# Kernel optimization log

Hardware: AMD Instinct MI355X
Metric: run time of the kernel (lower is better)

## Reference

```python
import jax, jax.numpy as jnp
import numpy as np

B, N, C, DK, TOPK = 4, 4096, 256, 64, 8


def setup_inputs() -> dict:
    key = jax.random.key(0)
    k1, k2, k3 = jax.random.split(key, 3)
    x = jax.random.normal(k1, (B, N, C), dtype=jnp.float32)
    # nn.Linear(channels, d_k, bias=False) weights, stored as [C, DK] for x @ W
    W_q = jax.random.normal(k2, (C, DK), dtype=jnp.float32) * (C ** -0.5)
    W_k = jax.random.normal(k3, (C, DK), dtype=jnp.float32) * (C ** -0.5)
    return {"x": x, "W_q": W_q, "W_k": W_k, "top_k": TOPK}


def reference(x, W_q, W_k, top_k):
    d_k = W_q.shape[-1]
    scale = d_k ** -0.5
    Q = x @ W_q                                   # [B, N, DK]
    K = x @ W_k                                   # [B, N, DK]
    S = jnp.einsum('bnd,bmd->bnm', Q, K) * scale  # [B, N, N]
    _, topk_idx = jax.lax.top_k(S, top_k)         # [B, N, top_k]
    n = S.shape[-1]
    # scatter True at top-k column indices per row (mirrors torch scatter_)
    row_mask = lambda idx: jnp.zeros((n,), dtype=bool).at[idx].set(True)
    mask = jax.vmap(jax.vmap(row_mask))(topk_idx)  # [B, N, N] bool
    S_masked = jnp.where(mask, S, -jnp.inf)
    A = jax.nn.softmax(S_masked, axis=-1)
    return A
```

## Files before the change

### kernel.cpp

```cpp
#include <hip/hip_runtime.h>
#include <math.h>

#define NROW 16384
#define NCOL 4096
#define CDIM 256
#define DKDIM 64
#define SCALE 0.125f

typedef float v4f __attribute__((ext_vector_type(4)));
typedef __attribute__((ext_vector_type(8))) short short8v;
typedef __attribute__((ext_vector_type(4))) float f32x4;

__device__ __forceinline__ unsigned mono(float v) {
  unsigned u = __float_as_uint(v);
  unsigned s = (unsigned)(((int)u) >> 31);
  return u ^ (s | 0x80000000u);
}
__device__ __forceinline__ float unmono(unsigned k) {
  unsigned u = (k & 0x80000000u) ? (k ^ 0x80000000u) : ~k;
  return __uint_as_float(u);
}
__device__ __forceinline__ unsigned short f2bf(float f) {
  unsigned u = __float_as_uint(f);
  u += 0x7FFFu + ((u >> 16) & 1u);
  return (unsigned short)(u >> 16);
}
__device__ __forceinline__ unsigned umaxu(unsigned a, unsigned b) { return a > b ? a : b; }

__device__ __forceinline__ void ins8(unsigned tk[8], unsigned& tmin, int& tmpos, unsigned v) {
  #pragma unroll
  for (int j = 0; j < 8; ++j) if (j == tmpos) tk[j] = v;
  tmin = tk[0]; tmpos = 0;
  #pragma unroll
  for (int j = 1; j < 8; ++j) if (tk[j] < tmin) { tmin = tk[j]; tmpos = j; }
}
__device__ __forceinline__ unsigned umax8(const unsigned kv[8]) {
  unsigned a = umaxu(umaxu(kv[0], kv[1]), umaxu(kv[2], kv[3]));
  unsigned b = umaxu(umaxu(kv[4], kv[5]), umaxu(kv[6], kv[7]));
  return umaxu(a, b);
}
__device__ __forceinline__ void seed8(const unsigned* __restrict__ sp,
                                      unsigned tk[8], unsigned& tmin, int& tmpos) {
  uint4 ka = *(const uint4*)(sp);
  uint4 kb = *(const uint4*)(sp + 4);
  tk[0] = ka.x; tk[1] = ka.y; tk[2] = ka.z; tk[3] = ka.w;
  tk[4] = kb.x; tk[5] = kb.y; tk[6] = kb.z; tk[7] = kb.w;
  tmin = tk[0]; tmpos = 0;
  #pragma unroll
  for (int j = 1; j < 8; ++j) if (tk[j] < tmin) { tmin = tk[j]; tmpos = j; }
}
__device__ __forceinline__ void scan8(const unsigned* __restrict__ sp,
                                      unsigned tk[8], unsigned& tmin, int& tmpos) {
  uint4 ka = *(const uint4*)(sp);
  uint4 kb = *(const uint4*)(sp + 4);
  unsigned kv[8] = {ka.x, ka.y, ka.z, ka.w, kb.x, kb.y, kb.z, kb.w};
  unsigned gm = umax8(kv);
  #pragma unroll
  for (int pass = 0; pass < 2; ++pass) {
    if (__any(gm > tmin)) {
      if (gm > tmin) {
        ins8(tk, tmin, tmpos, gm);
        #pragma unroll
        for (int j = 0; j < 8; ++j) if (kv[j] == gm) kv[j] = 0u;
      }
      gm = umax8(kv);
    }
  }
  if (__any(gm > tmin)) {
    #pragma unroll
    for (int j = 0; j < 8; ++j) if (kv[j] > tmin) ins8(tk, tmin, tmpos, kv[j]);
  }
}

__global__ __launch_bounds__(512, 2) void qk_proj(
    const float* __restrict__ x, const float* __restrict__ Wq,
    const float* __restrict__ Wk, float* __restrict__ Qt,
    float* __restrict__ Kt, unsigned short* __restrict__ Qh,
    unsigned short* __restrict__ Kh) {
  __shared__ float4 xs4[64][65];
  const int t = threadIdx.x;
  const int rb = blockIdx.x;
  {
    const float4* xg = (const float4*)(x + (size_t)rb * 64 * CDIM);
    #pragma unroll
    for (int i = 0; i < 8; ++i) {
      int idx = i * 512 + t;
      xs4[idx >> 6][idx & 63] = xg[idx];
    }
  }
  __syncthreads();

  const int lane = t & 63;
  const int wu = __builtin_amdgcn_readfirstlane(t >> 6);
  const int proj = wu >> 2;
  const int chunk = wu & 3;
  const float* __restrict__ Wp = proj ? Wk : Wq;

  float acc[16];
  #pragma unroll
  for (int j = 0; j < 16; ++j) acc[j] = 0.f;

  #pragma unroll 4
  for (int cs = 0; cs < 64; ++cs) {
    float4 xv = xs4[lane][cs];
    const float xc[4] = {xv.x, xv.y, xv.z, xv.w};
    #pragma unroll
    for (int i = 0; i < 4; ++i) {
      const float4* __restrict__ w4 =
          (const float4*)(Wp + (size_t)(cs * 4 + i) * DKDIM + chunk * 16);
      float4 wa = w4[0], wb = w4[1], wc = w4[2], wd = w4[3];
      float xi = xc[i];
      acc[0]  = fmaf(xi, wa.x, acc[0]);  acc[1]  = fmaf(xi, wa.y, acc[1]);
      acc[2]  = fmaf(xi, wa.z, acc[2]);  acc[3]  = fmaf(xi, wa.w, acc[3]);
      acc[4]  = fmaf(xi, wb.x, acc[4]);  acc[5]  = fmaf(xi, wb.y, acc[5]);
      acc[6]  = fmaf(xi, wb.z, acc[6]);  acc[7]  = fmaf(xi, wb.w, acc[7]);
      acc[8]  = fmaf(xi, wc.x, acc[8]);  acc[9]  = fmaf(xi, wc.y, acc[9]);
      acc[10] = fmaf(xi, wc.z, acc[10]); acc[11] = fmaf(xi, wc.w, acc[11]);
      acc[12] = fmaf(xi, wd.x, acc[12]); acc[13] = fmaf(xi, wd.y, acc[13]);
      acc[14] = fmaf(xi, wd.z, acc[14]); acc[15] = fmaf(xi, wd.w, acc[15]);
    }
  }

  const int gr = rb * 64 + lane;
  float* Of = (proj ? Kt : Qt) + (size_t)gr * 64 + chunk * 16;
  #pragma unroll
  for (int i = 0; i < 4; ++i) {
    float4 o = {acc[4 * i], acc[4 * i + 1], acc[4 * i + 2], acc[4 * i + 3]};
    ((float4*)Of)[i] = o;
  }
  unsigned short* Oh = (proj ? Kh : Qh) + (size_t)gr * 64 + chunk * 16;
  unsigned hp[8];
  #pragma unroll
  for (int i = 0; i < 8; ++i)
    hp[i] = (unsigned)f2bf(acc[2 * i]) | ((unsigned)f2bf(acc[2 * i + 1]) << 16);
  uint4 h0 = {hp[0], hp[1], hp[2], hp[3]};
  uint4 h1 = {hp[4], hp[5], hp[6], hp[7]};
  ((uint4*)Oh)[0] = h0;
  ((uint4*)Oh)[1] = h1;
}

__global__ __launch_bounds__(256, 4) void s_cand(
    const unsigned short* __restrict__ Qh, const unsigned short* __restrict__ Kh,
    float* __restrict__ out, unsigned* __restrict__ wsk) {
  __shared__ unsigned keys[4][16 * 132];
  const int t = threadIdx.x;
  const int lane = t & 63;
  const int w = __builtin_amdgcn_readfirstlane(t >> 6);
  const int f = blockIdx.x;
  const int xs = f & 7;
  const int i5 = f >> 3;
  const int combo = xs * 4 + (i5 >> 6);
  const int rbL = i5 & 63;
  const int b = combo >> 3;
  const int chunk = combo & 7;
  const int rb = b * 64 + rbL;

  const int l15 = lane & 15, lk = lane >> 4;
  const int rowg = (b << 12) + rbL * 64 + w * 16 + l15;
  const short8v a0 = *(const short8v*)(Qh + (size_t)rowg * 64 + lk * 8);
  const short8v a1 = *(const short8v*)(Qh + (size_t)rowg * 64 + lk * 8 + 32);

  {
    v4f z = {0.f, 0.f, 0.f, 0.f};
    v4f* o4 = (v4f*)out + (size_t)rb * 64 * 1024 + chunk * 128;
    #pragma unroll 8
    for (int i = 0; i < 32; ++i) {
      int g = i * 256 + t;
      __builtin_nontemporal_store(z, &o4[(size_t)(g >> 7) * 1024 + (g & 127)]);
    }
  }

  unsigned* krow = keys[w];
  const int myrow = lane >> 2, q = lane & 3;
  const unsigned short* Kb = Kh + ((size_t)(b << 12)) * 64;

  unsigned tk[8]; unsigned tmin; int tmpos;

  #pragma unroll 1
  for (int qt = 0; qt < 4; ++qt) {
    const int colbase = chunk * 512 + qt * 128;
    #pragma unroll
    for (int ct = 0; ct < 8; ++ct) {
      const int col = colbase + ct * 16 + l15;
      const unsigned short* kp = Kb + (size_t)col * 64 + lk * 8;
      const short8v b0 = *(const short8v*)(kp);
      const short8v b1 = *(const short8v*)(kp + 32);
      f32x4 acc = {0.f, 0.f, 0.f, 0.f};
      acc = __builtin_amdgcn_mfma_f32_16x16x32_bf16(a0, b0, acc, 0, 0, 0);
      acc = __builtin_amdgcn_mfma_f32_16x16x32_bf16(a1, b1, acc, 0, 0, 0);
      #pragma unroll
      for (int i = 0; i < 4; ++i) {
        unsigned kk = (mono(acc[i]) & 0xFFFFF000u) | (unsigned)col;
        krow[(lk * 4 + i) * 132 + ct * 16 + l15] = kk;
      }
    }
    const unsigned* sp = krow + myrow * 132 + q * 32;
    if (qt == 0) {
      seed8(sp, tk, tmin, tmpos);
      scan8(sp + 8, tk, tmin, tmpos);
      scan8(sp + 16, tk, tmin, tmpos);
      scan8(sp + 24, tk, tmin, tmpos);
    } else {
      #pragma unroll
      for (int g = 0; g < 4; ++g) scan8(sp + 8 * g, tk, tmin, tmpos);
    }
  }

  {
    uint4 s0 = {tk[0], tk[1], tk[2], tk[3]};
    uint4 s1 = {tk[4], tk[5], tk[6], tk[7]};
    uint4* mp4 = (uint4*)(krow + myrow * 36 + q * 8);
    mp4[0] = s0; mp4[1] = s1;
  }
  if (lane < 16) {
    const unsigned* mp = krow + lane * 36;
    unsigned mt[8]; unsigned mmin; int mmpos;
    seed8(mp, mt, mmin, mmpos);
    scan8(mp + 8, mt, mmin, mmpos);
    scan8(mp + 16, mt, mmin, mmpos);
    scan8(mp + 24, mt, mmin, mmpos);
    const int grow = (b << 12) + rbL * 64 + w * 16 + lane;
    uint4 o0 = {mt[0], mt[1], mt[2], mt[3]};
    uint4 o1 = {mt[4], mt[5], mt[6], mt[7]};
    uint4* wp = (uint4*)(wsk + (size_t)grow * 64 + chunk * 8);
    wp[0] = o0; wp[1] = o1;
  }
}

__global__ __launch_bounds__(256) void finalize(
    const float* __restrict__ Qt, const float* __restrict__ Kt,
    const unsigned* __restrict__ wsk, float* __restrict__ out) {
  const int t = threadIdx.x;
  const int lane = t & 63;
  const int w = t >> 6;
  const int row = blockIdx.x * 4 + w;
  const int b = row >> 12;
  const unsigned key = wsk[(size_t)row * 64 + lane];
  const int col = (int)(key & 0xFFFu);
  const float4* Kp = (const float4*)(Kt + ((size_t)((b << 12) + col)) * 64);
  const float4* Qp = (const float4*)(Qt + (size_t)row * 64);
  float s = 0.f;
  #pragma unroll
  for (int g = 0; g < 16; ++g) {
    float4 qf = Qp[g];
    float4 kf = Kp[g];
    s = fmaf(qf.x, kf.x, s);
    s = fmaf(qf.y, kf.y, s);
    s = fmaf(qf.z, kf.z, s);
    s = fmaf(qf.w, kf.w, s);
  }
  unsigned kx = mono(s);
  float vals[8]; int cols[8];
  #pragma unroll
  for (int it = 0; it < 8; ++it) {
    unsigned m = kx;
    #pragma unroll
    for (int d = 1; d < 64; d <<= 1) m = umaxu(m, (unsigned)__shfl_xor((int)m, d, 64));
    unsigned long long win = __ballot(kx == m);
    int wl = (int)__ffsll(win) - 1;
    cols[it] = __shfl(col, wl, 64);
    vals[it] = unmono(m);
    if (lane == wl) kx = 0u;
  }
  float e[8], sum = 0.f;
  #pragma unroll
  for (int it = 0; it < 8; ++it) { e[it] = __expf((vals[it] - vals[0]) * SCALE); sum += e[it]; }
  float inv = 1.f / sum;
  if (lane == 0) {
    float* orow = out + ((size_t)row << 12);
    #pragma unroll
    for (int it = 0; it < 8; ++it) orow[cols[it]] = e[it] * inv;
  }
}

extern "C" void kernel_launch(void* const* d_in, const int* in_sizes, int n_in,
                              void* d_out, int out_size, void* d_ws, size_t ws_size,
                              hipStream_t stream) {
  const float* x  = (const float*)d_in[0];
  const float* Wq = (const float*)d_in[1];
  const float* Wk = (const float*)d_in[2];
  float* out = (float*)d_out;

  char* ws = (char*)d_ws;
  float* Qt = (float*)ws;
  float* Kt = (float*)(ws + ((size_t)4 << 20));
  unsigned short* Qh = (unsigned short*)(ws + ((size_t)8 << 20));
  unsigned short* Kh = (unsigned short*)(ws + ((size_t)10 << 20));
  unsigned* wsk = (unsigned*)(ws + ((size_t)12 << 20));

  qk_proj<<<dim3(NROW / 64), 512, 0, stream>>>(x, Wq, Wk, Qt, Kt, Qh, Kh);
  s_cand<<<2048, 256, 0, stream>>>(Qh, Kh, out, wsk);
  finalize<<<NROW / 4, 256, 0, stream>>>(Qt, Kt, wsk, out);
}
```

Measured before the change: 467.9 us.

## Move output zero-fill into projection kernel and keep top-k candidates in registers

The zero-fill of the 256MB output moves from the candidate kernel into the projection kernel, where it is interleaved with the FMA loop. The idea is that the write traffic overlaps compute in a kernel that is not bandwidth-bound. The candidate kernel now keeps per-row top-8 state in registers for each of the 4 MFMA output rows, instead of staging every score key through LDS and scanning. A two-level LDS merge follows at the end. The cost is higher register pressure in s_cand, and qk_proj becomes dominated by the fill.

```diff
diff --git a/kernel.cpp b/kernel.cpp
--- a/kernel.cpp
+++ b/kernel.cpp
@@ -39,21 +39,19 @@
   unsigned b = umaxu(umaxu(kv[4], kv[5]), umaxu(kv[6], kv[7]));
   return umaxu(a, b);
 }
-__device__ __forceinline__ void seed8(const unsigned* __restrict__ sp,
-                                      unsigned tk[8], unsigned& tmin, int& tmpos) {
-  uint4 ka = *(const uint4*)(sp);
-  uint4 kb = *(const uint4*)(sp + 4);
-  tk[0] = ka.x; tk[1] = ka.y; tk[2] = ka.z; tk[3] = ka.w;
-  tk[4] = kb.x; tk[5] = kb.y; tk[6] = kb.z; tk[7] = kb.w;
+__device__ __forceinline__ void seed8r(const unsigned kv[8],
+                                       unsigned tk[8], unsigned& tmin, int& tmpos) {
+  #pragma unroll
+  for (int j = 0; j < 8; ++j) tk[j] = kv[j];
   tmin = tk[0]; tmpos = 0;
   #pragma unroll
   for (int j = 1; j < 8; ++j) if (tk[j] < tmin) { tmin = tk[j]; tmpos = j; }
 }
-__device__ __forceinline__ void scan8(const unsigned* __restrict__ sp,
-                                      unsigned tk[8], unsigned& tmin, int& tmpos) {
-  uint4 ka = *(const uint4*)(sp);
-  uint4 kb = *(const uint4*)(sp + 4);
-  unsigned kv[8] = {ka.x, ka.y, ka.z, ka.w, kb.x, kb.y, kb.z, kb.w};
+__device__ __forceinline__ void scan8r(const unsigned kvin[8],
+                                       unsigned tk[8], unsigned& tmin, int& tmpos) {
+  unsigned kv[8];
+  #pragma unroll
+  for (int j = 0; j < 8; ++j) kv[j] = kvin[j];
   unsigned gm = umax8(kv);
   #pragma unroll
   for (int pass = 0; pass < 2; ++pass) {
@@ -71,12 +69,26 @@
     for (int j = 0; j < 8; ++j) if (kv[j] > tmin) ins8(tk, tmin, tmpos, kv[j]);
   }
 }
+__device__ __forceinline__ void seed8(const unsigned* __restrict__ sp,
+                                      unsigned tk[8], unsigned& tmin, int& tmpos) {
+  uint4 ka = *(const uint4*)(sp);
+  uint4 kb = *(const uint4*)(sp + 4);
+  unsigned kv[8] = {ka.x, ka.y, ka.z, ka.w, kb.x, kb.y, kb.z, kb.w};
+  seed8r(kv, tk, tmin, tmpos);
+}
+__device__ __forceinline__ void scan8(const unsigned* __restrict__ sp,
+                                      unsigned tk[8], unsigned& tmin, int& tmpos) {
+  uint4 ka = *(const uint4*)(sp);
+  uint4 kb = *(const uint4*)(sp + 4);
+  unsigned kv[8] = {ka.x, ka.y, ka.z, ka.w, kb.x, kb.y, kb.z, kb.w};
+  scan8r(kv, tk, tmin, tmpos);
+}
 
 __global__ __launch_bounds__(512, 2) void qk_proj(
     const float* __restrict__ x, const float* __restrict__ Wq,
     const float* __restrict__ Wk, float* __restrict__ Qt,
     float* __restrict__ Kt, unsigned short* __restrict__ Qh,
-    unsigned short* __restrict__ Kh) {
+    unsigned short* __restrict__ Kh, float* __restrict__ out) {
   __shared__ float4 xs4[64][65];
   const int t = threadIdx.x;
   const int rb = blockIdx.x;
@@ -96,12 +108,20 @@
   const int chunk = wu & 3;
   const float* __restrict__ Wp = proj ? Wk : Wq;
 
+  v4f* __restrict__ ofill = (v4f*)out + (size_t)rb * 65536;
+  const v4f z = {0.f, 0.f, 0.f, 0.f};
+
   float acc[16];
   #pragma unroll
   for (int j = 0; j < 16; ++j) acc[j] = 0.f;
 
   #pragma unroll 4
   for (int cs = 0; cs < 64; ++cs) {
+    {
+      int g0 = cs * 1024 + t;
+      __builtin_nontemporal_store(z, &ofill[g0]);
+      __builtin_nontemporal_store(z, &ofill[g0 + 512]);
+    }
     float4 xv = xs4[lane][cs];
     const float xc[4] = {xv.x, xv.y, xv.z, xv.w};
     #pragma unroll
@@ -141,7 +161,7 @@
 
 __global__ __launch_bounds__(256, 4) void s_cand(
     const unsigned short* __restrict__ Qh, const unsigned short* __restrict__ Kh,
-    float* __restrict__ out, unsigned* __restrict__ wsk) {
+    unsigned* __restrict__ wsk) {
   __shared__ unsigned keys[4][16 * 132];
   const int t = threadIdx.x;
   const int lane = t & 63;
@@ -153,35 +173,23 @@
   const int rbL = i5 & 63;
   const int b = combo >> 3;
   const int chunk = combo & 7;
-  const int rb = b * 64 + rbL;
 
   const int l15 = lane & 15, lk = lane >> 4;
   const int rowg = (b << 12) + rbL * 64 + w * 16 + l15;
   const short8v a0 = *(const short8v*)(Qh + (size_t)rowg * 64 + lk * 8);
   const short8v a1 = *(const short8v*)(Qh + (size_t)rowg * 64 + lk * 8 + 32);
 
-  {
-    v4f z = {0.f, 0.f, 0.f, 0.f};
-    v4f* o4 = (v4f*)out + (size_t)rb * 64 * 1024 + chunk * 128;
-    #pragma unroll 8
-    for (int i = 0; i < 32; ++i) {
-      int g = i * 256 + t;
-      __builtin_nontemporal_store(z, &o4[(size_t)(g >> 7) * 1024 + (g & 127)]);
-    }
-  }
-
-  unsigned* krow = keys[w];
-  const int myrow = lane >> 2, q = lane & 3;
   const unsigned short* Kb = Kh + ((size_t)(b << 12)) * 64;
 
-  unsigned tk[8]; unsigned tmin; int tmpos;
+  unsigned tk[4][8]; unsigned tmin[4]; int tmpos[4];
 
   #pragma unroll 1
-  for (int qt = 0; qt < 4; ++qt) {
-    const int colbase = chunk * 512 + qt * 128;
-    #pragma unroll
-    for (int ct = 0; ct < 8; ++ct) {
-      const int col = colbase + ct * 16 + l15;
+  for (int g = 0; g < 4; ++g) {
+    unsigned kv[4][8];
+    #pragma unroll
+    for (int t8 = 0; t8 < 8; ++t8) {
+      const int ct = g * 8 + t8;
+      const int col = chunk * 512 + ct * 16 + l15;
       const unsigned short* kp = Kb + (size_t)col * 64 + lk * 8;
       const short8v b0 = *(const short8v*)(kp);
       const short8v b1 = *(const short8v*)(kp + 32);
@@ -189,39 +197,51 @@
       acc = __builtin_amdgcn_mfma_f32_16x16x32_bf16(a0, b0, acc, 0, 0, 0);
       acc = __builtin_amdgcn_mfma_f32_16x16x32_bf16(a1, b1, acc, 0, 0, 0);
       #pragma unroll
-      for (int i = 0; i < 4; ++i) {
-        unsigned kk = (mono(acc[i]) & 0xFFFFF000u) | (unsigned)col;
-        krow[(lk * 4 + i) * 132 + ct * 16 + l15] = kk;
-      }
-    }
-    const unsigned* sp = krow + myrow * 132 + q * 32;
-    if (qt == 0) {
-      seed8(sp, tk, tmin, tmpos);
-      scan8(sp + 8, tk, tmin, tmpos);
-      scan8(sp + 16, tk, tmin, tmpos);
-      scan8(sp + 24, tk, tmin, tmpos);
+      for (int i = 0; i < 4; ++i)
+        kv[i][t8] = (mono(acc[i]) & 0xFFFFF000u) | (unsigned)col;
+    }
+    if (g == 0) {
+      #pragma unroll
+      for (int i = 0; i < 4; ++i) seed8r(kv[i], tk[i], tmin[i], tmpos[i]);
     } else {
       #pragma unroll
-      for (int g = 0; g < 4; ++g) scan8(sp + 8 * g, tk, tmin, tmpos);
-    }
-  }
-
+      for (int i = 0; i < 4; ++i) scan8r(kv[i], tk[i], tmin[i], tmpos[i]);
+    }
+  }
+
+  unsigned* krow = keys[w];
+  #pragma unroll
+  for (int i = 0; i < 4; ++i) {
+    uint4 s0 = {tk[i][0], tk[i][1], tk[i][2], tk[i][3]};
+    uint4 s1 = {tk[i][4], tk[i][5], tk[i][6], tk[i][7]};
+    uint4* mp4 = (uint4*)(krow + (lk * 4 + i) * 132 + l15 * 8);
+    mp4[0] = s0; mp4[1] = s1;
+  }
+  const int myrow = lane >> 2, q = lane & 3;
+  unsigned mt[8]; unsigned mmin; int mmpos;
   {
-    uint4 s0 = {tk[0], tk[1], tk[2], tk[3]};
-    uint4 s1 = {tk[4], tk[5], tk[6], tk[7]};
+    const unsigned* sp = krow + myrow * 132 + q * 32;
+    seed8(sp, mt, mmin, mmpos);
+    scan8(sp + 8, mt, mmin, mmpos);
+    scan8(sp + 16, mt, mmin, mmpos);
+    scan8(sp + 24, mt, mmin, mmpos);
+  }
+  {
+    uint4 s0 = {mt[0], mt[1], mt[2], mt[3]};
+    uint4 s1 = {mt[4], mt[5], mt[6], mt[7]};
     uint4* mp4 = (uint4*)(krow + myrow * 36 + q * 8);
     mp4[0] = s0; mp4[1] = s1;
   }
   if (lane < 16) {
     const unsigned* mp = krow + lane * 36;
-    unsigned mt[8]; unsigned mmin; int mmpos;
-    seed8(mp, mt, mmin, mmpos);
-    scan8(mp + 8, mt, mmin, mmpos);
-    scan8(mp + 16, mt, mmin, mmpos);
-    scan8(mp + 24, mt, mmin, mmpos);
+    unsigned ft[8]; unsigned fmin; int fmpos;
+    seed8(mp, ft, fmin, fmpos);
+    scan8(mp + 8, ft, fmin, fmpos);
+    scan8(mp + 16, ft, fmin, fmpos);
+    scan8(mp + 24, ft, fmin, fmpos);
     const int grow = (b << 12) + rbL * 64 + w * 16 + lane;
-    uint4 o0 = {mt[0], mt[1], mt[2], mt[3]};
-    uint4 o1 = {mt[4], mt[5], mt[6], mt[7]};
+    uint4 o0 = {ft[0], ft[1], ft[2], ft[3]};
+    uint4 o1 = {ft[4], ft[5], ft[6], ft[7]};
     uint4* wp = (uint4*)(wsk + (size_t)grow * 64 + chunk * 8);
     wp[0] = o0; wp[1] = o1;
   }
@@ -288,7 +308,7 @@
   unsigned short* Kh = (unsigned short*)(ws + ((size_t)10 << 20));
   unsigned* wsk = (unsigned*)(ws + ((size_t)12 << 20));
 
-  qk_proj<<<dim3(NROW / 64), 512, 0, stream>>>(x, Wq, Wk, Qt, Kt, Qh, Kh);
-  s_cand<<<2048, 256, 0, stream>>>(Qh, Kh, out, wsk);
+  qk_proj<<<dim3(NROW / 64), 512, 0, stream>>>(x, Wq, Wk, Qt, Kt, Qh, Kh, out);
+  s_cand<<<2048, 256, 0, stream>>>(Qh, Kh, wsk);
   finalize<<<NROW / 4, 256, 0, stream>>>(Qt, Kt, wsk, out);
 }
```

Measured after the change: 510.0 us. +9.0%, slower.
